# Optimization experiments

Hardware: AMD Instinct MI355X
Metric: run time of the kernel (lower is better)

Reference implementation:

```python
import jax, jax.numpy as jnp
import numpy as np

B = 64
NS = [5024, 1257, 315, 80, 21]  # padded vertex counts per mesh level
K = 9                            # spiral length
LAT = 256


def _sconv(x, idx, W, b, elu=True):
    # x: [B, N, F], idx: [N, K] spiral neighbor indices -> gather, GEMM, activation, zero-pad mask
    Bq, N, _ = x.shape
    g = x[:, idx.reshape(-1), :].reshape(Bq, N, -1)  # [B, N, K*F]
    o = g @ W + b
    if elu:
        o = jax.nn.elu(o)
    return o.at[:, -1, :].set(0.0)  # zero the padding vertex


def _pool(M, x):
    # M: [M_out, M_in] dense down/up-sample matrix
    return jnp.einsum('mn,bnf->bmf', M, x)


def _forward(x, s0, s1, s2, s3, D0, D1, D2, D3, U0, U1, U2, U3,
             We0, be0, We1, be1, We2, be2, We3, be3,
             fceW, fceb, fcdW, fcdb,
             Wd0, bd0, Wd1, bd1, Wd2, bd2, Wd3, bd3):
    # encoder: spiral conv + downsample at each level
    h = _pool(D0, _sconv(x, s0, We0, be0))
    h = _pool(D1, _sconv(h, s1, We1, be1))
    h = _pool(D2, _sconv(h, s2, We2, be2))
    h = _pool(D3, _sconv(h, s3, We3, be3))
    z = h.reshape(h.shape[0], -1) @ fceW + fceb          # [B, LAT]
    # decoder: upsample + spiral conv, last conv has identity activation
    h = (z @ fcdW + fcdb).reshape(z.shape[0], NS[4], -1)  # [B, 21, 256]
    h = _sconv(_pool(U3, h), s3, Wd0, bd0)
    h = _sconv(_pool(U2, h), s2, Wd1, bd1)
    h = _sconv(_pool(U1, h), s1, Wd2, bd2)
    h = _sconv(_pool(U0, h), s0, Wd3, bd3, elu=False)
    return h  # [B, 5024, 3]


def setup_inputs() -> dict:
    key = jax.random.key(0)
    ks = iter(jax.random.split(key, 64))
    nrm = lambda shape, s=0.05: jax.random.normal(next(ks), shape, dtype=jnp.float32) * s
    d = {}
    d['x'] = jax.random.normal(next(ks), (B, NS[0], 3), dtype=jnp.float32)
    for i in range(4):
        n = NS[i]
        d[f's{i}'] = jax.random.randint(next(ks), (n, K), 0, n, dtype=jnp.int32).astype(jnp.int64)
    for i in range(4):
        d[f'D{i}'] = nrm((NS[i + 1], NS[i]))
        d[f'U{i}'] = nrm((NS[i], NS[i + 1]))
    enc = [(3, 64), (64, 64), (64, 128), (128, 256)]
    for i, (fi, fo) in enumerate(enc):
        d[f'We{i}'] = nrm((fi * K, fo))
        d[f'be{i}'] = jnp.zeros((fo,), jnp.float32)
    d['fceW'] = nrm((NS[4] * 256, LAT))
    d['fceb'] = jnp.zeros((LAT,), jnp.float32)
    d['fcdW'] = nrm((LAT, NS[4] * 256))
    d['fcdb'] = jnp.zeros((NS[4] * 256,), jnp.float32)
    dec = [(256, 128), (128, 64), (64, 64), (64, 3)]
    for i, (fi, fo) in enumerate(dec):
        d[f'Wd{i}'] = nrm((fi * K, fo))
        d[f'bd{i}'] = jnp.zeros((fo,), jnp.float32)
    return d


def reference(x, s0, s1, s2, s3, D0, D1, D2, D3, U0, U1, U2, U3,
              We0, be0, We1, be1, We2, be2, We3, be3,
              fceW, fceb, fcdW, fcdb,
              Wd0, bd0, Wd1, bd1, Wd2, bd2, Wd3, bd3):
    return _forward(x, s0, s1, s2, s3, D0, D1, D2, D3, U0, U1, U2, U3,
                    We0, be0, We1, be1, We2, be2, We3, be3,
                    fceW, fceb, fcdW, fcdb,
                    Wd0, bd0, Wd1, bd1, Wd2, bd2, Wd3, bd3)
```

## Files before the change

### kernel.cpp

```cpp
#include <hip/hip_runtime.h>
#include <math.h>

typedef __attribute__((ext_vector_type(8))) _Float16 half8;
typedef __attribute__((ext_vector_type(4))) float f32x4;
typedef unsigned long long u64;

#define BK 32

#define EPI_NAT  0
#define EPI_TR   1
#define EPI_FCD  2
#define EPI_OUT  3
#define EPI_PART 4

typedef const __attribute__((address_space(1))) void* gas1;
typedef __attribute__((address_space(3))) void* las3;

__device__ __forceinline__ void gl16(const void* g, void* l) {
    __builtin_amdgcn_global_load_lds((gas1)g, (las3)l, 16, 0, 0);
}
template<int N> __device__ __forceinline__ void vwait() {
    asm volatile("s_waitcnt vmcnt(%0)" :: "n"(N) : "memory");
}
__device__ __forceinline__ void barx() {
    asm volatile("" ::: "memory");
    __builtin_amdgcn_s_barrier();
    asm volatile("" ::: "memory");
}

__global__ __launch_bounds__(256, 3) void pool4_k(
    const _Float16* __restrict__ Aw, const _Float16* __restrict__ Bw,
    _Float16* __restrict__ Cp, int M, int Np, u64 c_rs)
{
    constexpr int LPS = 6;

    __shared__ _Float16 sA[2][64][64];
    __shared__ _Float16 sB[2][128][64];

    const int t  = threadIdx.x;
    const int m0 = blockIdx.y * 64;
    const int f0 = blockIdx.x * 128;
    const int lane = t & 63;
    const int wid  = t >> 6;
    const int wm = wid >> 1;
    const int wf = wid & 1;
    const int lm = lane & 15;
    const int lg = lane >> 4;

    f32x4 acc[2][4];
    #pragma unroll
    for (int i = 0; i < 2; ++i)
        #pragma unroll
        for (int j = 0; j < 4; ++j)
            acc[i][j] = (f32x4)0.0f;

    auto stage = [&](int buf, int ks) {
        #pragma unroll
        for (int j = 0; j < 2; ++j) {
            int c   = t + j * 256;
            int row = c >> 3;
            int ch  = (c & 7) ^ (row & 7);
            int rc  = m0 + row; if (rc >= M) rc = M - 1;
            gl16(Aw + (u64)rc * Np + ks * 64 + ch * 8,
                 (_Float16*)&sA[buf][0][0] + (u64)c * 8);
        }
        #pragma unroll
        for (int j = 0; j < 4; ++j) {
            int c   = t + j * 256;
            int row = c >> 3;
            int ch  = (c & 7) ^ (row & 7);
            gl16(Bw + (u64)(f0 + row) * Np + ks * 64 + ch * 8,
                 (_Float16*)&sB[buf][0][0] + (u64)c * 8);
        }
    };

    auto compute = [&](int buf) {
        #pragma unroll
        for (int kh = 0; kh < 2; ++kh) {
            const int ch = (kh * 4 + lg) ^ (lm & 7);
            half8 af[2], bf[4];
            #pragma unroll
            for (int i = 0; i < 2; ++i)
                af[i] = *(const half8*)&sA[buf][wm * 32 + i * 16 + lm][ch * 8];
            #pragma unroll
            for (int j = 0; j < 4; ++j)
                bf[j] = *(const half8*)&sB[buf][wf * 64 + j * 16 + lm][ch * 8];
            #pragma unroll
            for (int i = 0; i < 2; ++i)
                #pragma unroll
                for (int j = 0; j < 4; ++j)
                    acc[i][j] = __builtin_amdgcn_mfma_f32_16x16x32_f16(af[i], bf[j], acc[i][j], 0, 0, 0);
        }
    };

    const int ke = Np / 64;
    stage(0, 0);
    if (1 < ke) stage(1, 1);
    for (int ks = 0; ks < ke; ++ks) {
        if (ke - ks >= 2) vwait<LPS>();
        else              vwait<0>();
        barx();
        compute(ks & 1);
        barx();
        if (ks + 2 < ke) stage(ks & 1, ks + 2);
    }

    #pragma unroll
    for (int j = 0; j < 4; ++j) {
        int fl = f0 + wf * 64 + j * 16 + lm;
        #pragma unroll
        for (int i = 0; i < 2; ++i) {
            #pragma unroll
            for (int r = 0; r < 4; ++r) {
                int m = m0 + wm * 32 + i * 16 + lg * 4 + r;
                if (m < M)
                    Cp[(u64)m * c_rs + fl] = (_Float16)acc[i][j][r];
            }
        }
    }
}

template<int TBM>
__global__ __launch_bounds__(256, 3) void pool2_k(
    const _Float16* __restrict__ Aw, const _Float16* __restrict__ Bw,
    _Float16* __restrict__ Cp, int M, int Np, u64 c_rs)
{
    constexpr int FM  = TBM / 32;
    constexpr int LPS = TBM / 64 + 2;

    __shared__ _Float16 sA[3][TBM][BK];
    __shared__ _Float16 sB[3][128][BK];

    const int t  = threadIdx.x;
    const int m0 = blockIdx.y * TBM;
    const int f0 = blockIdx.x * 128;
    const int lane = t & 63;
    const int wid  = t >> 6;
    const int wm = wid >> 1;
    const int wf = wid & 1;
    const int lm = lane & 15;
    const int lg = lane >> 4;

    f32x4 acc[FM][4];
    #pragma unroll
    for (int i = 0; i < FM; ++i)
        #pragma unroll
        for (int j = 0; j < 4; ++j)
            acc[i][j] = (f32x4)0.0f;

    auto stage = [&](int buf, int ks) {
        #pragma unroll
        for (int j = 0; j < TBM / 64; ++j) {
            int c   = t + j * 256;
            int row = c >> 2;
            int sw  = ((c & 3) ^ ((row >> 1) & 3)) * 8;
            int rc  = m0 + row; if (rc >= M) rc = M - 1;
            gl16(Aw + (u64)rc * Np + ks * BK + sw,
                 (_Float16*)&sA[buf][0][0] + (u64)c * 8);
        }
        #pragma unroll
        for (int j = 0; j < 2; ++j) {
            int c   = t + j * 256;
            int row = c >> 2;
            int sw  = ((c & 3) ^ ((row >> 1) & 3)) * 8;
            gl16(Bw + (u64)(f0 + row) * Np + ks * BK + sw,
                 (_Float16*)&sB[buf][0][0] + (u64)c * 8);
        }
    };

    auto compute = [&](int buf) {
        const int sa = (lg ^ ((lm >> 1) & 3)) * 8;
        half8 af[FM], bf[4];
        #pragma unroll
        for (int i = 0; i < FM; ++i)
            af[i] = *(const half8*)&sA[buf][wm * (FM * 16) + i * 16 + lm][sa];
        #pragma unroll
        for (int j = 0; j < 4; ++j)
            bf[j] = *(const half8*)&sB[buf][wf * 64 + j * 16 + lm][sa];
        #pragma unroll
        for (int i = 0; i < FM; ++i)
            #pragma unroll
            for (int j = 0; j < 4; ++j)
                acc[i][j] = __builtin_amdgcn_mfma_f32_16x16x32_f16(af[i], bf[j], acc[i][j], 0, 0, 0);
    };

    const int ke = Np / BK;
    stage(0, 0);
    if (1 < ke) stage(1, 1);
    if (2 < ke) stage(2, 2);
    int cur = 0;
    for (int ks = 0; ks < ke; ++ks) {
        int rem = ke - ks;
        if (rem >= 3)      vwait<2 * LPS>();
        else if (rem == 2) vwait<LPS>();
        else               vwait<0>();
        barx();
        compute(cur);
        barx();
        if (ks + 3 < ke) stage(cur, ks + 3);
        cur = (cur == 2) ? 0 : cur + 1;
    }

    #pragma unroll
    for (int j = 0; j < 4; ++j) {
        int fl = f0 + wf * 64 + j * 16 + lm;
        #pragma unroll
        for (int i = 0; i < FM; ++i) {
            #pragma unroll
            for (int r = 0; r < 4; ++r) {
                int m = m0 + wm * (FM * 16) + i * 16 + lg * 4 + r;
                if (m < M)
                    Cp[(u64)m * c_rs + fl] = (_Float16)acc[i][j][r];
            }
        }
    }
}

template<int AMODE, int EPI, int TBM, int TBF, int WM, int WF>
__global__ __launch_bounds__(256) void gemm_k(
    const _Float16* __restrict__ Aw, u64 a_rs,
    const int* __restrict__ idx, int FiLog,
    const _Float16* __restrict__ Bw,
    const float* __restrict__ bias,
    void* __restrict__ Cp, u64 c_rs, int Mp_out,
    int M, int Np, int F, int flags, int ksp)
{
    constexpr int FM = TBM / WM / 16;
    constexpr int FF = TBF / WF / 16;
    constexpr int LPS_A = TBM / 64;
    constexpr bool BSM = (TBF < 64);
    constexpr int LPS_B = BSM ? 0 : TBF / 64;
    constexpr int LW0 = LPS_A + (BSM ? 1 : LPS_B);
    constexpr int LWX = LPS_A + LPS_B;
    constexpr int NI = (AMODE == 1) ? TBM : 2;

    __shared__ _Float16 sA[3][TBM][BK];
    __shared__ _Float16 sB[3][TBF][BK];
    __shared__ int sIdx[NI][9];

    const int t  = threadIdx.x;
    const int b  = blockIdx.z;
    const int m0 = blockIdx.y * TBM;
    const int f0 = blockIdx.x * TBF;
    const int lane = t & 63;
    const int wid  = t >> 6;
    const int wm = wid / WF;
    const int wf = wid % WF;
    const int lm = lane & 15;
    const int lg = lane >> 4;
    const int Fi = 1 << FiLog;

    f32x4 acc[FM][FF];
    #pragma unroll
    for (int i = 0; i < FM; ++i)
        #pragma unroll
        for (int j = 0; j < FF; ++j)
            acc[i][j] = (f32x4)0.0f;

    if constexpr (AMODE == 1) {
        for (int i = t; i < TBM * 9; i += 256) {
            int r = i / 9, k = i - r * 9;
            int rc = m0 + r; if (rc >= M) rc = M - 1;
            sIdx[r][k] = idx[rc * 9 + k];
        }
        __syncthreads();
    } else if constexpr (AMODE == 5) {
        if (t < 18) {
            int r = t / 9, k = t - r * 9;
            sIdx[r][k] = idx[((m0 >> 6) + r) * 9 + k];
        }
        __syncthreads();
    }

    auto stage = [&](int buf, int ks) {
        if constexpr (AMODE != 2) {
            #pragma unroll
            for (int j = 0; j < LPS_A; ++j) {
                int c   = t + j * 256;
                int row = c >> 2;
                int sw  = ((c & 3) ^ ((row >> 1) & 3)) * 8;
                int col = ks * BK + sw;
                const _Float16* src;
                if constexpr (AMODE == 3) {
                    int rc = m0 + row; if (rc >= M) rc = M - 1;
                    src = Aw + (u64)rc * Np + col;
                } else if constexpr (AMODE == 1) {
                    int k = col >> FiLog, fi = col & (Fi - 1);
                    src = Aw + (u64)sIdx[row][k] * a_rs + b * Fi + fi;
                } else if constexpr (AMODE == 4) {
                    int k = col >> FiLog, fi = col & (Fi - 1);
                    src = Aw + (u64)k * a_rs + (m0 + row) * Fi + fi;
                } else {
                    int k = col >> FiLog, fi = col & (Fi - 1);
                    int bb = (m0 + row) & 63;
                    src = Aw + (u64)sIdx[row >> 6][k] * a_rs + bb * Fi + fi;
                }
                gl16(src, &sA[buf][row][(c & 3) * 8]);
            }
        }
        if constexpr (!BSM) {
            #pragma unroll
            for (int j = 0; j < LPS_B; ++j) {
                int c   = t + j * 256;
                int row = c >> 2;
                int sw  = ((c & 3) ^ ((row >> 1) & 3)) * 8;
                gl16(Bw + (u64)(f0 + row) * Np + ks * BK + sw, &sB[buf][row][(c & 3) * 8]);
            }
        } else {
            if (wid == 0) {
                int c   = t;
                int row = c >> 2;
                int sw  = ((c & 3) ^ ((row >> 1) & 3)) * 8;
                gl16(Bw + (u64)(f0 + row) * Np + ks * BK + sw, &sB[buf][row][(c & 3) * 8]);
            }
        }
    };

    auto compute = [&](int buf) {
        const int sa = (lg ^ ((lm >> 1) & 3)) * 8;
        half8 af[FM], bf[FF];
        #pragma unroll
        for (int i = 0; i < FM; ++i)
            af[i] = *(const half8*)&sA[buf][wm * (FM * 16) + i * 16 + lm][sa];
        #pragma unroll
        for (int j = 0; j < FF; ++j)
            bf[j] = *(const half8*)&sB[buf][wf * (FF * 16) + j * 16 + lm][sa];
        #pragma unroll
        for (int i = 0; i < FM; ++i)
            #pragma unroll
            for (int j = 0; j < FF; ++j)
                acc[i][j] = __builtin_amdgcn_mfma_f32_16x16x32_f16(af[i], bf[j], acc[i][j], 0, 0, 0);
    };

    if constexpr (AMODE == 2) {
        stage(0, 0);
        {
            int row = t >> 1;
            int base = (t & 1) * 16;
            int rg = m0 + row;
            #pragma unroll
            for (int q = 0; q < 16; ++q) {
                int n = base + q;
                _Float16 val = (_Float16)0.f;
                if (rg < M && n < 27) {
                    int k = n / 3, fi = n - k * 3;
                    val = Aw[(u64)idx[rg * 9 + k] * a_rs + b * 3 + fi];
                }
                int ch = (n >> 3) ^ ((row >> 1) & 3);
                sA[0][row][ch * 8 + (n & 7)] = val;
            }
        }
        __syncthreads();
        compute(0);
    } else {
        int kb = 0, ke = Np / BK;
        if constexpr (AMODE == 4) { kb = b * ksp; ke = kb + ksp; }
        stage(0, kb);
        if (kb + 1 < ke) stage(1, kb + 1);
        if (kb + 2 < ke) stage(2, kb + 2);
        int cur = 0;
        for (int ks = kb; ks < ke; ++ks) {
            int rem = ke - ks;
            if (rem >= 3) {
                if constexpr (LW0 == LWX) vwait<2 * LW0>();
                else { if (wid == 0) vwait<2 * LW0>(); else vwait<2 * LWX>(); }
            } else if (rem == 2) {
                if constexpr (LW0 == LWX) vwait<LW0>();
                else { if (wid == 0) vwait<LW0>(); else vwait<LWX>(); }
            } else {
                vwait<0>();
            }
            barx();
            compute(cur);
            barx();
            if (ks + 3 < ke) stage(cur, ks + 3);
            cur = (cur == 2) ? 0 : cur + 1;
        }
    }

    #pragma unroll
    for (int j = 0; j < FF; ++j) {
        int fl = f0 + wf * (FF * 16) + j * 16 + lm;
        float bv = 0.f;
        if (bias != nullptr && fl < F) bv = bias[fl];
        #pragma unroll
        for (int i = 0; i < FM; ++i) {
            #pragma unroll
            for (int r = 0; r < 4; ++r) {
                int m = m0 + wm * (FM * 16) + i * 16 + lg * 4 + r;
                float v = acc[i][j][r] + bv;
                if (flags & 1) v = (v > 0.f) ? v : expm1f(v);
                if constexpr (EPI == EPI_NAT) {
                    if (m < M && fl < F)
                        ((_Float16*)Cp)[(u64)m * c_rs + fl] = (_Float16)v;
                } else if constexpr (EPI == EPI_TR) {
                    if (m < Mp_out && fl < F) {
                        float o = (m < M && !((flags & 2) && m == M - 1)) ? v : 0.f;
                        ((_Float16*)Cp)[(u64)b * c_rs + (u64)fl * Mp_out + m] = (_Float16)o;
                    }
                } else if constexpr (EPI == EPI_FCD) {
                    if (m < M && fl < F)
                        ((_Float16*)Cp)[((u64)m * 256 + (fl & 255)) * 32 + (fl >> 8)] = (_Float16)v;
                } else if constexpr (EPI == EPI_PART) {
                    if (m < M && fl < F)
                        ((float*)Cp)[(u64)b * c_rs + (u64)m * F + fl] = v;
                } else {
                    if (m < M && fl < F) {
                        int vo = m >> 6, bb = m & 63;
                        float o = ((flags & 2) && vo == Mp_out - 1) ? 0.f : v;
                        ((float*)Cp)[((u64)bb * Mp_out + vo) * 3 + fl] = o;
                    }
                }
            }
        }
    }
}

struct CvtPtrs { const float* p[18]; };

constexpr int CV_R[18]  = {1257,5024,315,1257,80,315,21,80,  64,64,128,256,256,5376,128,64,64,16};
constexpr int CV_N[18]  = {5024,1257,1257,315,315,80,80,21,  27,576,576,1152,5376,256,2304,1152,576,576};
constexpr int CV_NP[18] = {5120,1280,1280,320,320,96,96,32,  32,576,576,1152,5376,256,2304,1152,576,576};
constexpr int CV_F[18]  = {0,0,0,0,0,0,0,0,  64,64,128,256,256,5376,128,64,64,3};

constexpr u64 cv_elems(int i) { return (u64)CV_R[i] * CV_NP[i]; }
constexpr u64 cv_off(int i) { u64 o = 0; for (int j = 0; j < i; ++j) o += (cv_elems(j) + 255) & ~(u64)255; return o; }
constexpr int cv_blk(int i) { return (int)((cv_elems(i) + 255) >> 8); }
constexpr int cv_start(int i) { int s = 0; for (int j = 0; j < i; ++j) s += cv_blk(j); return s; }

__global__ __launch_bounds__(256) void cvt_all(CvtPtrs ps, _Float16* __restrict__ dst)
{
    const int bx = blockIdx.x, t = threadIdx.x;
    #pragma unroll
    for (int i = 0; i < 18; ++i) {
        if (bx >= cv_start(i) && bx < cv_start(i + 1)) {
            const u64 e = (u64)(bx - cv_start(i)) * 256 + t;
            if (e < cv_elems(i)) {
                const int NP = CV_NP[i], N = CV_N[i], Fo = CV_F[i];
                int row = (int)(e / (u64)NP);
                int col = (int)(e - (u64)row * NP);
                float v = 0.f;
                const float* s = ps.p[i];
                if (Fo == 0) { if (col < N) v = s[(u64)row * N + col]; }
                else         { if (col < N && row < Fo) v = s[(u64)col * Fo + row]; }
                dst[cv_off(i) + e] = (_Float16)v;
            }
        }
    }
}

__global__ void cvt_x(const float* __restrict__ src, _Float16* __restrict__ dst)
{
    int i = blockIdx.x * 256 + threadIdx.x;
    if (i >= 64 * 5024 * 3) return;
    int v = i / 192;
    int r = i - v * 192;
    int b = r / 3, c = r - b * 3;
    dst[i] = (_Float16)src[((u64)b * 5024 + v) * 3 + c];
}

__global__ void reduce_fce(const float* __restrict__ part, const float* __restrict__ bias,
                           _Float16* __restrict__ z)
{
    int i = blockIdx.x * 256 + threadIdx.x;
    int fl = i & 255;
    float s = bias[fl];
    #pragma unroll
    for (int p = 0; p < 8; ++p) s += part[(u64)p * 16384 + i];
    z[i] = (_Float16)s;
}

extern "C" void kernel_launch(void* const* d_in, const int* in_sizes, int n_in,
                              void* d_out, int out_size, void* d_ws, size_t ws_size,
                              hipStream_t stream)
{
    const float* x  = (const float*)d_in[0];
    const int* s0 = (const int*)d_in[1];
    const int* s1 = (const int*)d_in[2];
    const int* s2 = (const int*)d_in[3];
    const int* s3 = (const int*)d_in[4];
    const float* be0 = (const float*)d_in[14];
    const float* be1 = (const float*)d_in[16];
    const float* be2 = (const float*)d_in[18];
    const float* be3 = (const float*)d_in[20];
    const float* fceb = (const float*)d_in[22];
    const float* fcdb = (const float*)d_in[24];
    const float* bd0 = (const float*)d_in[26];
    const float* bd1 = (const float*)d_in[28];
    const float* bd2 = (const float*)d_in[30];
    const float* bd3 = (const float*)d_in[32];

    _Float16* W = (_Float16*)d_ws;
    size_t off = 0;
    auto alloc = [&](size_t e) { size_t o = off; off += (e + 255) & ~(size_t)255; return o; };

    const size_t oActV = alloc((size_t)5024 * 4096);
    const size_t oActT = alloc((size_t)4096 * 5120);
    const size_t oZ    = alloc((size_t)64 * 256);
    const size_t oPart = alloc((size_t)8 * 64 * 256 * 2);
    const size_t oU3in = alloc((size_t)16384 * 32);
    const size_t oXp   = alloc((size_t)5024 * 192);
    const size_t oCvt  = alloc((size_t)(cv_off(17) + ((cv_elems(17) + 255) & ~(u64)255)));
    auto wofs = [&](int i) { return oCvt + (size_t)cv_off(i); };

    cvt_x<<<dim3((64 * 5024 * 3 + 255) / 256), 256, 0, stream>>>(x, W + oXp);
    {
        CvtPtrs ps;
        ps.p[0] = (const float*)d_in[5];
        ps.p[1] = (const float*)d_in[6];
        ps.p[2] = (const float*)d_in[7];
        ps.p[3] = (const float*)d_in[8];
        ps.p[4] = (const float*)d_in[9];
        ps.p[5] = (const float*)d_in[10];
        ps.p[6] = (const float*)d_in[11];
        ps.p[7] = (const float*)d_in[12];
        ps.p[8] = (const float*)d_in[13];
        ps.p[9] = (const float*)d_in[15];
        ps.p[10] = (const float*)d_in[17];
        ps.p[11] = (const float*)d_in[19];
        ps.p[12] = (const float*)d_in[21];
        ps.p[13] = (const float*)d_in[23];
        ps.p[14] = (const float*)d_in[25];
        ps.p[15] = (const float*)d_in[27];
        ps.p[16] = (const float*)d_in[29];
        ps.p[17] = (const float*)d_in[31];
        cvt_all<<<dim3(cv_start(18)), 256, 0, stream>>>(ps, W + oCvt);
    }
    hipMemsetAsync(W + oU3in, 0, (size_t)16384 * 32 * sizeof(_Float16), stream);

    #define GEMM(AM, EP, BM_, BF_, WM_, WF_, gx, gy, gz, Aw_, ars_, idx_, FiL_, Bw_, bias_, Cp_, crs_, Mp_, M_, Np_, F_, fl_, ksp_) \
        gemm_k<AM, EP, BM_, BF_, WM_, WF_><<<dim3(gx, gy, gz), 256, 0, stream>>>( \
            Aw_, ars_, idx_, FiL_, Bw_, bias_, Cp_, crs_, Mp_, M_, Np_, F_, fl_, ksp_)
    #define POOL(TBM_, gx, gy, Aw_, Bw_, Cp_, M_, Np_, crs_) \
        pool2_k<TBM_><<<dim3(gx, gy), 256, 0, stream>>>(Aw_, Bw_, Cp_, M_, Np_, crs_)
    #define POOL4(gx, gy, Aw_, Bw_, Cp_, M_, Np_, crs_) \
        pool4_k<<<dim3(gx, gy), 256, 0, stream>>>(Aw_, Bw_, Cp_, M_, Np_, crs_)

    GEMM(2, EPI_TR, 128, 64, 2, 2, 1, 40, 64, W + oXp, 192, s0, 0,
         W + wofs(8), be0, W + oActT, (u64)64 * 5120, 5120, 5024, 32, 64, 3, 0);
    POOL4(32, 20, W + wofs(0), W + oActT, W + oActV, 1257, 5120, 4096);
    GEMM(1, EPI_TR, 128, 64, 2, 2, 1, 10, 64, W + oActV, 4096, s1, 6,
         W + wofs(9), be1, W + oActT, (u64)64 * 1280, 1280, 1257, 576, 64, 3, 0);
    POOL(64, 32, 5, W + wofs(2), W + oActT, W + oActV, 315, 1280, 4096);
    GEMM(1, EPI_TR, 128, 64, 2, 2, 2, 3, 64, W + oActV, 4096, s2, 6,
         W + wofs(10), be2, W + oActT, (u64)128 * 320, 320, 315, 576, 128, 3, 0);
    POOL(64, 64, 2, W + wofs(4), W + oActT, W + oActV, 80, 320, 8192);
    GEMM(1, EPI_TR, 128, 64, 2, 2, 4, 1, 64, W + oActV, 8192, s3, 7,
         W + wofs(11), be3, W + oActT, (u64)256 * 96, 96, 80, 1152, 256, 3, 0);
    POOL(64, 128, 1, W + wofs(6), W + oActT, W + oActV, 21, 96, 16384);
    GEMM(4, EPI_PART, 64, 64, 2, 2, 4, 1, 8, W + oActV, 16384, nullptr, 8,
         W + wofs(12), nullptr, W + oPart, (u64)64 * 256, 0, 64, 5376, 256, 0, 21);
    reduce_fce<<<dim3(64), 256, 0, stream>>>((const float*)(W + oPart), fceb, W + oZ);
    GEMM(3, EPI_FCD, 64, 128, 2, 2, 42, 1, 1, W + oZ, 0, nullptr, 0,
         W + wofs(13), fcdb, W + oU3in, 0, 0, 64, 256, 5376, 0, 0);
    POOL(64, 128, 2, W + wofs(7), W + oU3in, W + oActV, 80, 32, 16384);
    GEMM(1, EPI_TR, 128, 64, 2, 2, 2, 1, 64, W + oActV, 16384, s3, 8,
         W + wofs(14), bd0, W + oActT, (u64)128 * 96, 96, 80, 2304, 128, 3, 0);
    POOL(64, 64, 5, W + wofs(5), W + oActT, W + oActV, 315, 96, 8192);
    GEMM(1, EPI_TR, 128, 64, 2, 2, 1, 3, 64, W + oActV, 8192, s2, 7,
         W + wofs(15), bd1, W + oActT, (u64)64 * 320, 320, 315, 1152, 64, 3, 0);
    POOL4(32, 20, W + wofs(3), W + oActT, W + oActV, 1257, 320, 4096);
    GEMM(1, EPI_TR, 128, 64, 2, 2, 1, 10, 64, W + oActV, 4096, s1, 6,
         W + wofs(16), bd2, W + oActT, (u64)64 * 1280, 1280, 1257, 576, 64, 3, 0);
    POOL4(32, 79, W + wofs(1), W + oActT, W + oActV, 5024, 1280, 4096);
    GEMM(5, EPI_OUT, 128, 16, 4, 1, 1, 2512, 1, W + oActV, 4096, s0, 6,
         W + wofs(17), bd3, d_out, 0, 5024, 321536, 576, 3, 2, 0);
    #undef GEMM
    #undef POOL
    #undef POOL4
}
```

Baseline: 552.8 us.

## Pad first-layer input to 4 channels for vector gathers and vectorize transposed stores

Pads the input vertex features from 3 to 4 fp16 channels per batch, and matches that with a reordered first-layer weight matrix padded to K=64. The first spiral conv can then gather each neighbor with one 8-byte load, using spiral indices cached in shared memory, and runs two MFMA k-steps instead of one. The transposed epilogue now writes four consecutive vertices with one half4 store instead of four scalar stores. The cost is doing twice the MFMA work on the zero-padded K for layer 0, plus a larger input buffer.

After: 505.8 us. -8.5%, faster.

```diff
diff --git a/kernel.cpp b/kernel.cpp
--- a/kernel.cpp
+++ b/kernel.cpp
@@ -2,6 +2,7 @@
 #include <math.h>
 
 typedef __attribute__((ext_vector_type(8))) _Float16 half8;
+typedef __attribute__((ext_vector_type(4))) _Float16 half4;
 typedef __attribute__((ext_vector_type(4))) float f32x4;
 typedef unsigned long long u64;
 
@@ -232,7 +233,7 @@
     constexpr int LPS_B = BSM ? 0 : TBF / 64;
     constexpr int LW0 = LPS_A + (BSM ? 1 : LPS_B);
     constexpr int LWX = LPS_A + LPS_B;
-    constexpr int NI = (AMODE == 1) ? TBM : 2;
+    constexpr int NI = (AMODE == 1 || AMODE == 2) ? TBM : 2;
 
     __shared__ _Float16 sA[3][TBM][BK];
     __shared__ _Float16 sB[3][TBF][BK];
@@ -257,7 +258,7 @@
         for (int j = 0; j < FF; ++j)
             acc[i][j] = (f32x4)0.0f;
 
-    if constexpr (AMODE == 1) {
+    if constexpr (AMODE == 1 || AMODE == 2) {
         for (int i = t; i < TBM * 9; i += 256) {
             int r = i / 9, k = i - r * 9;
             int rc = m0 + r; if (rc >= M) rc = M - 1;
@@ -334,24 +335,29 @@
 
     if constexpr (AMODE == 2) {
         stage(0, 0);
+        stage(1, 1);
         {
             int row = t >> 1;
-            int base = (t & 1) * 16;
-            int rg = m0 + row;
-            #pragma unroll
-            for (int q = 0; q < 16; ++q) {
-                int n = base + q;
-                _Float16 val = (_Float16)0.f;
-                if (rg < M && n < 27) {
-                    int k = n / 3, fi = n - k * 3;
-                    val = Aw[(u64)idx[rg * 9 + k] * a_rs + b * 3 + fi];
-                }
-                int ch = (n >> 3) ^ ((row >> 1) & 3);
-                sA[0][row][ch * 8 + (n & 7)] = val;
-            }
-        }
+            int h   = t & 1;
+            #pragma unroll
+            for (int cc = 0; cc < 4; ++cc) {
+                int g0 = h * 8 + cc * 2;
+                int g1 = g0 + 1;
+                half4 lo = {(_Float16)0,(_Float16)0,(_Float16)0,(_Float16)0};
+                half4 hi = lo;
+                if (g0 < 9) lo = *(const half4*)(Aw + (u64)sIdx[row][g0] * a_rs + b * 4);
+                if (g1 < 9) hi = *(const half4*)(Aw + (u64)sIdx[row][g1] * a_rs + b * 4);
+                half8 w;
+                #pragma unroll
+                for (int q = 0; q < 4; ++q) { w[q] = lo[q]; w[4 + q] = hi[q]; }
+                int cp = cc ^ ((row >> 1) & 3);
+                *(half8*)&sA[h][row][cp * 8] = w;
+            }
+        }
+        vwait<0>();
         __syncthreads();
         compute(0);
+        compute(1);
     } else {
         int kb = 0, ke = Np / BK;
         if constexpr (AMODE == 4) { kb = b * ksp; ke = kb + ksp; }
@@ -378,37 +384,55 @@
         }
     }
 
-    #pragma unroll
-    for (int j = 0; j < FF; ++j) {
-        int fl = f0 + wf * (FF * 16) + j * 16 + lm;
-        float bv = 0.f;
-        if (bias != nullptr && fl < F) bv = bias[fl];
-        #pragma unroll
-        for (int i = 0; i < FM; ++i) {
-            #pragma unroll
-            for (int r = 0; r < 4; ++r) {
-                int m = m0 + wm * (FM * 16) + i * 16 + lg * 4 + r;
-                float v = acc[i][j][r] + bv;
-                if (flags & 1) v = (v > 0.f) ? v : expm1f(v);
-                if constexpr (EPI == EPI_NAT) {
-                    if (m < M && fl < F)
-                        ((_Float16*)Cp)[(u64)m * c_rs + fl] = (_Float16)v;
-                } else if constexpr (EPI == EPI_TR) {
-                    if (m < Mp_out && fl < F) {
-                        float o = (m < M && !((flags & 2) && m == M - 1)) ? v : 0.f;
-                        ((_Float16*)Cp)[(u64)b * c_rs + (u64)fl * Mp_out + m] = (_Float16)o;
+    if constexpr (EPI == EPI_TR) {
+        #pragma unroll
+        for (int j = 0; j < FF; ++j) {
+            int fl = f0 + wf * (FF * 16) + j * 16 + lm;
+            float bv = (bias != nullptr && fl < F) ? bias[fl] : 0.f;
+            #pragma unroll
+            for (int i = 0; i < FM; ++i) {
+                int mb = m0 + wm * (FM * 16) + i * 16 + lg * 4;
+                if (fl < F && mb < Mp_out) {
+                    half4 o;
+                    #pragma unroll
+                    for (int r = 0; r < 4; ++r) {
+                        int m = mb + r;
+                        float v = acc[i][j][r] + bv;
+                        if (flags & 1) v = (v > 0.f) ? v : expm1f(v);
+                        o[r] = (m < M && !((flags & 2) && m == M - 1)) ? (_Float16)v : (_Float16)0.f;
                     }
-                } else if constexpr (EPI == EPI_FCD) {
-                    if (m < M && fl < F)
-                        ((_Float16*)Cp)[((u64)m * 256 + (fl & 255)) * 32 + (fl >> 8)] = (_Float16)v;
-                } else if constexpr (EPI == EPI_PART) {
-                    if (m < M && fl < F)
-                        ((float*)Cp)[(u64)b * c_rs + (u64)m * F + fl] = v;
-                } else {
-                    if (m < M && fl < F) {
-                        int vo = m >> 6, bb = m & 63;
-                        float o = ((flags & 2) && vo == Mp_out - 1) ? 0.f : v;
-                        ((float*)Cp)[((u64)bb * Mp_out + vo) * 3 + fl] = o;
+                    *(half4*)&((_Float16*)Cp)[(u64)b * c_rs + (u64)fl * Mp_out + mb] = o;
+                }
+            }
+        }
+    } else {
+        #pragma unroll
+        for (int j = 0; j < FF; ++j) {
+            int fl = f0 + wf * (FF * 16) + j * 16 + lm;
+            float bv = 0.f;
+            if (bias != nullptr && fl < F) bv = bias[fl];
+            #pragma unroll
+            for (int i = 0; i < FM; ++i) {
+                #pragma unroll
+                for (int r = 0; r < 4; ++r) {
+                    int m = m0 + wm * (FM * 16) + i * 16 + lg * 4 + r;
+                    float v = acc[i][j][r] + bv;
+                    if (flags & 1) v = (v > 0.f) ? v : expm1f(v);
+                    if constexpr (EPI == EPI_NAT) {
+                        if (m < M && fl < F)
+                            ((_Float16*)Cp)[(u64)m * c_rs + fl] = (_Float16)v;
+                    } else if constexpr (EPI == EPI_FCD) {
+                        if (m < M && fl < F)
+                            ((_Float16*)Cp)[((u64)m * 256 + (fl & 255)) * 32 + (fl >> 8)] = (_Float16)v;
+                    } else if constexpr (EPI == EPI_PART) {
+                        if (m < M && fl < F)
+                            ((float*)Cp)[(u64)b * c_rs + (u64)m * F + fl] = v;
+                    } else {
+                        if (m < M && fl < F) {
+                            int vo = m >> 6, bb = m & 63;
+                            float o = ((flags & 2) && vo == Mp_out - 1) ? 0.f : v;
+                            ((float*)Cp)[((u64)bb * Mp_out + vo) * 3 + fl] = o;
+                        }
                     }
                 }
             }
@@ -420,7 +444,7 @@
 
 constexpr int CV_R[18]  = {1257,5024,315,1257,80,315,21,80,  64,64,128,256,256,5376,128,64,64,16};
 constexpr int CV_N[18]  = {5024,1257,1257,315,315,80,80,21,  27,576,576,1152,5376,256,2304,1152,576,576};
-constexpr int CV_NP[18] = {5120,1280,1280,320,320,96,96,32,  32,576,576,1152,5376,256,2304,1152,576,576};
+constexpr int CV_NP[18] = {5120,1280,1280,320,320,96,96,32,  64,576,576,1152,5376,256,2304,1152,576,576};
 constexpr int CV_F[18]  = {0,0,0,0,0,0,0,0,  64,64,128,256,256,5376,128,64,64,3};
 
 constexpr u64 cv_elems(int i) { return (u64)CV_R[i] * CV_NP[i]; }
@@ -441,8 +465,14 @@
                 int col = (int)(e - (u64)row * NP);
                 float v = 0.f;
                 const float* s = ps.p[i];
-                if (Fo == 0) { if (col < N) v = s[(u64)row * N + col]; }
-                else         { if (col < N && row < Fo) v = s[(u64)col * Fo + row]; }
+                if (i == 8) {
+                    int k = col >> 2, c = col & 3;
+                    if (c < 3 && k < 9) v = s[(u64)(k * 3 + c) * Fo + row];
+                } else if (Fo == 0) {
+                    if (col < N) v = s[(u64)row * N + col];
+                } else {
+                    if (col < N && row < Fo) v = s[(u64)col * Fo + row];
+                }
                 dst[cv_off(i) + e] = (_Float16)v;
             }
         }
@@ -452,11 +482,11 @@
 __global__ void cvt_x(const float* __restrict__ src, _Float16* __restrict__ dst)
 {
     int i = blockIdx.x * 256 + threadIdx.x;
-    if (i >= 64 * 5024 * 3) return;
-    int v = i / 192;
-    int r = i - v * 192;
-    int b = r / 3, c = r - b * 3;
-    dst[i] = (_Float16)src[((u64)b * 5024 + v) * 3 + c];
+    if (i >= 5024 * 256) return;
+    int v = i >> 8;
+    int r = i & 255;
+    int b = r >> 2, c = r & 3;
+    dst[i] = (c < 3) ? (_Float16)src[((u64)b * 5024 + v) * 3 + c] : (_Float16)0.f;
 }
 
 __global__ void reduce_fce(const float* __restrict__ part, const float* __restrict__ bias,
@@ -499,11 +529,11 @@
     const size_t oZ    = alloc((size_t)64 * 256);
     const size_t oPart = alloc((size_t)8 * 64 * 256 * 2);
     const size_t oU3in = alloc((size_t)16384 * 32);
-    const size_t oXp   = alloc((size_t)5024 * 192);
+    const size_t oXp   = alloc((size_t)5024 * 256);
     const size_t oCvt  = alloc((size_t)(cv_off(17) + ((cv_elems(17) + 255) & ~(u64)255)));
     auto wofs = [&](int i) { return oCvt + (size_t)cv_off(i); };
 
-    cvt_x<<<dim3((64 * 5024 * 3 + 255) / 256), 256, 0, stream>>>(x, W + oXp);
+    cvt_x<<<dim3(5024), 256, 0, stream>>>(x, W + oXp);
     {
         CvtPtrs ps;
         ps.p[0] = (const float*)d_in[5];
@@ -536,8 +566,8 @@
     #define POOL4(gx, gy, Aw_, Bw_, Cp_, M_, Np_, crs_) \
         pool4_k<<<dim3(gx, gy), 256, 0, stream>>>(Aw_, Bw_, Cp_, M_, Np_, crs_)
 
-    GEMM(2, EPI_TR, 128, 64, 2, 2, 1, 40, 64, W + oXp, 192, s0, 0,
-         W + wofs(8), be0, W + oActT, (u64)64 * 5120, 5120, 5024, 32, 64, 3, 0);
+    GEMM(2, EPI_TR, 128, 64, 2, 2, 1, 40, 64, W + oXp, 256, s0, 0,
+         W + wofs(8), be0, W + oActT, (u64)64 * 5120, 5120, 5024, 64, 64, 3, 0);
     POOL4(32, 20, W + wofs(0), W + oActT, W + oActV, 1257, 5120, 4096);
     GEMM(1, EPI_TR, 128, 64, 2, 2, 1, 10, 64, W + oActV, 4096, s1, 6,
          W + wofs(9), be1, W + oActT, (u64)64 * 1280, 1280, 1257, 576, 64, 3, 0);
```
